# Performance work log

Hardware: AMD Instinct MI355X
Metric: run time of the kernel (lower is better)

The kernel has to match this reference:

```python
import jax, jax.numpy as jnp
import numpy as np

NUM_HEADS = 16
NUM_KV_HEADS = 4
HEAD_DIM = 64
HIDDEN = 1024
B, S = 2, 2048


def setup_inputs() -> dict:
    key = jax.random.key(0)
    ks = jax.random.split(key, 9)
    sc = 0.02
    return {
        "x": jax.random.normal(ks[0], (B, S, HIDDEN), dtype=jnp.float32),
        "Wq": jax.random.normal(ks[1], (HIDDEN, NUM_HEADS * HEAD_DIM), dtype=jnp.float32) * sc,
        "bq": jnp.zeros((NUM_HEADS * HEAD_DIM,), dtype=jnp.float32),
        "Wk": jax.random.normal(ks[2], (HIDDEN, NUM_KV_HEADS * HEAD_DIM), dtype=jnp.float32) * sc,
        "bk": jnp.zeros((NUM_KV_HEADS * HEAD_DIM,), dtype=jnp.float32),
        "Wv": jax.random.normal(ks[3], (HIDDEN, NUM_KV_HEADS * HEAD_DIM), dtype=jnp.float32) * sc,
        "bv": jnp.zeros((NUM_KV_HEADS * HEAD_DIM,), dtype=jnp.float32),
        "Wo": jax.random.normal(ks[4], (NUM_HEADS * HEAD_DIM, HIDDEN), dtype=jnp.float32) * sc,
        "bo": jnp.zeros((HIDDEN,), dtype=jnp.float32),
    }


def reference(x, Wq, bq, Wk, bk, Wv, bv, Wo, bo):
    bs, seq, _ = x.shape
    groups = NUM_HEADS // NUM_KV_HEADS
    # projections -> [B, H, S, D]
    q = (x @ Wq + bq).reshape(bs, seq, NUM_HEADS, HEAD_DIM).transpose(0, 2, 1, 3)
    k = (x @ Wk + bk).reshape(bs, seq, NUM_KV_HEADS, HEAD_DIM).transpose(0, 2, 1, 3)
    v = (x @ Wv + bv).reshape(bs, seq, NUM_KV_HEADS, HEAD_DIM).transpose(0, 2, 1, 3)
    # repeat_interleave KV heads to match query heads (GQA expansion)
    k = jnp.repeat(k, groups, axis=1)
    v = jnp.repeat(v, groups, axis=1)
    # NOTE: source applies NO 1/sqrt(d) scaling and no mask/ALiBi
    scores = jnp.einsum("bhqd,bhkd->bhqk", q, k)
    attn = jax.nn.softmax(scores.astype(jnp.float32), axis=-1).astype(q.dtype)
    out = jnp.einsum("bhqk,bhkd->bhqd", attn, v)
    out = out.transpose(0, 2, 1, 3).reshape(bs, seq, NUM_HEADS * HEAD_DIM)
    return out @ Wo + bo
```

## Files before the change

### kernel.cpp

```cpp
#include <hip/hip_runtime.h>

#define NHEADS 16
#define NKV    4
#define HDIM   64
#define HIDDEN 1024
#define BATCH  2
#define SEQ    2048
#define MROWS  (BATCH * SEQ)
#define LOG2E  1.44269504088896340736f

typedef __bf16 bf16_t;
typedef bf16_t bf16x8 __attribute__((ext_vector_type(8)));
typedef float  f32x4  __attribute__((ext_vector_type(4)));

template<int N>  struct ic { static constexpr int  v = N; };
template<bool B> struct bc { static constexpr bool v = B; };

__device__ __forceinline__ float bf2f(unsigned short u) {
    return __uint_as_float(((unsigned int)u) << 16);
}
__device__ __forceinline__ unsigned short f2bf(float f) {
    unsigned int u = __float_as_uint(f);
    u += 0x7FFFu + ((u >> 16) & 1u);
    return (unsigned short)(u >> 16);
}

__device__ __forceinline__ void gld16(const unsigned short* g, unsigned short* l)
{
    __builtin_amdgcn_global_load_lds(
        (const __attribute__((address_space(1))) void*)g,
        (__attribute__((address_space(3))) void*)l,
        16, 0, 0);
}

__device__ __forceinline__ int swz(int row, int ch) {
    return (row * 8 + (ch ^ (row & 7))) * 8;
}

__device__ __forceinline__ bool sniff_is_f32(const unsigned short* __restrict__ x)
{
    const int e = (x[threadIdx.x & 63] >> 7) & 0xFF;
    const unsigned long long ok = __ballot(e >= 110 && e <= 140);
    return __popcll(ok) < 56;
}

__device__ __forceinline__ void load8cvt(const void* base, size_t elem, bool isf32, unsigned short out[8])
{
    if (!isf32) {
        *(uint4*)out = *(const uint4*)((const unsigned short*)base + elem);
    } else {
        const float* p = (const float*)base + elem;
        float4 v0 = *(const float4*)p;
        float4 v1 = *(const float4*)(p + 4);
        out[0] = f2bf(v0.x); out[1] = f2bf(v0.y); out[2] = f2bf(v0.z); out[3] = f2bf(v0.w);
        out[4] = f2bf(v1.x); out[5] = f2bf(v1.y); out[6] = f2bf(v1.z); out[7] = f2bf(v1.w);
    }
}
__device__ __forceinline__ float bias_at(const void* b, int i, bool isf32)
{
    return isf32 ? ((const float*)b)[i] : bf2f(((const unsigned short*)b)[i]);
}

__global__ __launch_bounds__(256)
void prep_kernel(const void* __restrict__ x,
                 const void* __restrict__ Wq, const void* __restrict__ Wk,
                 const void* __restrict__ Wv, const void* __restrict__ Wo,
                 unsigned short* __restrict__ xb,
                 unsigned short* __restrict__ Wqkvt,
                 unsigned short* __restrict__ Wot)
{
    const bool isf32 = sniff_is_f32((const unsigned short*)x);
    const int t = threadIdx.x;
    int bid = blockIdx.x;

    if (bid < 2048) {
        if (!isf32) return;
        const size_t c = (size_t)bid * 256 + t;
        unsigned short v[8];
        load8cvt(x, c * 8, true, v);
        *(uint4*)(&xb[c * 8]) = *(uint4*)v;
        return;
    }
    bid -= 2048;
    const void* src; unsigned short* dst; int N, rowoff;
    if (bid < 256)      {             src = Wq; dst = Wqkvt; N = 1024; rowoff = 0;    }
    else if (bid < 320) { bid -= 256; src = Wk; dst = Wqkvt; N = 256;  rowoff = 1024; }
    else if (bid < 384) { bid -= 320; src = Wv; dst = Wqkvt; N = 256;  rowoff = 1280; }
    else                { bid -= 384; src = Wo; dst = Wot;   N = 1024; rowoff = 0;    }
    const int ntx = N / 64;
    const int gn0 = (bid % ntx) * 64;
    const int gk0 = (bid / ntx) * 64;

    __shared__ unsigned short Ts[64][72];
#pragma unroll
    for (int half = 0; half < 2; ++half) {
        const int kl = (t >> 3) + half * 32;
        const int n8 = (t & 7) * 8;
        unsigned short v[8];
        load8cvt(src, (size_t)(gk0 + kl) * N + gn0 + n8, isf32, v);
        *(uint4*)(&Ts[kl][n8]) = *(uint4*)v;
    }
    __syncthreads();
#pragma unroll
    for (int half = 0; half < 2; ++half) {
        const int nl = (t >> 3) + half * 32;
        const int k8 = (t & 7) * 8;
        unsigned short v[8];
#pragma unroll
        for (int j = 0; j < 8; ++j) v[j] = Ts[k8 + j][nl];
        *(uint4*)(&dst[(size_t)(rowoff + gn0 + nl) * HIDDEN + gk0 + k8]) = *(uint4*)v;
    }
}

template<int KK>
__device__ __forceinline__ void gemm_tile(const unsigned short* __restrict__ A,
                                          const unsigned short* __restrict__ Bt,
                                          int m0, int n0,
                                          unsigned short* As, unsigned short* Bs,
                                          f32x4 (&acc)[4][4])
{
    const int tid  = threadIdx.x;
    const int lane = tid & 63;
    const int wave = tid >> 6;
    const int quad = lane >> 4;
    const int l15  = lane & 15;
    const int wr   = wave >> 1;
    const int wc   = wave & 1;

    const int srow = tid >> 3;
    const int gch  = ((tid & 7) ^ (srow & 7)) * 8;

    const unsigned short* ga[4];
    const unsigned short* gb[4];
#pragma unroll
    for (int r = 0; r < 4; ++r) {
        ga[r] = A  + (size_t)(m0 + r * 32 + srow) * KK + gch;
        gb[r] = Bt + (size_t)(n0 + r * 32 + srow) * KK + gch;
    }
    unsigned short* const adst = As + wave * 512;
    unsigned short* const bdst = Bs + wave * 512;

    int aoffs[2][4], boffs[2][4];
#pragma unroll
    for (int kk = 0; kk < 2; ++kk) {
#pragma unroll
        for (int i = 0; i < 4; ++i) {
            aoffs[kk][i] = swz(wr * 64 + i * 16 + l15, kk * 4 + quad);
            boffs[kk][i] = swz(wc * 64 + i * 16 + l15, kk * 4 + quad);
        }
    }

#define GSTAGE(B)                                                     \
    do {                                                              \
        _Pragma("unroll")                                             \
        for (int r = 0; r < 4; ++r) {                                 \
            gld16(ga[r], adst + (B) * 8192 + r * 2048); ga[r] += 64;  \
            gld16(gb[r], bdst + (B) * 8192 + r * 2048); gb[r] += 64;  \
        }                                                             \
    } while (0)

    constexpr int nk = KK / 64;
    GSTAGE(0);
#pragma unroll 2
    for (int k = 0; k < nk; ++k) {
        const int cur = k & 1;
        __syncthreads();
        if (k + 1 < nk) GSTAGE(cur ^ 1);

#pragma unroll
        for (int kk = 0; kk < 2; ++kk) {
            bf16x8 af[4], bfv[4];
#pragma unroll
            for (int i = 0; i < 4; ++i) {
                af[i]  = *(const bf16x8*)(&As[cur * 8192 + aoffs[kk][i]]);
                bfv[i] = *(const bf16x8*)(&Bs[cur * 8192 + boffs[kk][i]]);
            }
            __builtin_amdgcn_s_setprio(1);
#pragma unroll
            for (int i = 0; i < 4; ++i)
#pragma unroll
                for (int j = 0; j < 4; ++j)
                    acc[i][j] = __builtin_amdgcn_mfma_f32_16x16x32_bf16(af[i], bfv[j], acc[i][j], 0, 0, 0);
            __builtin_amdgcn_s_setprio(0);
        }
    }
#undef GSTAGE
}

__global__ __launch_bounds__(256)
void gemm_qkv(const void* __restrict__ xraw,
              const unsigned short* __restrict__ xb,
              const unsigned short* __restrict__ Bt,
              const void* __restrict__ bq, const void* __restrict__ bk,
              const void* __restrict__ bv,
              unsigned short* __restrict__ Qh,
              unsigned short* __restrict__ Kh,
              unsigned short* __restrict__ Vt)
{
    __shared__ __align__(16) unsigned short As[2 * 128 * 64];
    __shared__ __align__(16) unsigned short Bs[2 * 128 * 64];
    const bool bias_f32 = sniff_is_f32((const unsigned short*)xraw);
    const unsigned short* A = bias_f32 ? xb : (const unsigned short*)xraw;
    const int lane = threadIdx.x & 63;
    const int wave = threadIdx.x >> 6;
    const int quad = lane >> 4, l15 = lane & 15;
    const int wr = wave >> 1, wc = wave & 1;
    const int m0 = blockIdx.y * 128, n0 = blockIdx.x * 128;

    f32x4 acc[4][4] = {};
    gemm_tile<HIDDEN>(A, Bt, m0, n0, As, Bs, acc);

#pragma unroll
    for (int i = 0; i < 4; ++i) {
#pragma unroll
        for (int j = 0; j < 4; ++j) {
            const int nn  = n0 + wc * 64 + j * 16 + l15;
            const int mmb = m0 + wr * 64 + i * 16 + quad * 4;
            const int b = mmb >> 11, s0 = mmb & 2047;
            if (nn < 1024) {
                const float bias = bias_at(bq, nn, bias_f32);
                const int h = nn >> 6, d = nn & 63;
                const size_t idx0 = (((size_t)(b * NHEADS + h)) * SEQ + s0) * 64 + d;
#pragma unroll
                for (int r = 0; r < 4; ++r)
                    Qh[idx0 + (size_t)r * 64] = f2bf((acc[i][j][r] + bias) * LOG2E);
            } else if (nn < 1280) {
                const int nk = nn - 1024;
                const float bias = bias_at(bk, nk, bias_f32);
                const int h = nk >> 6, d = nk & 63;
                const size_t idx0 = (((size_t)(b * NKV + h)) * SEQ + s0) * 64 + d;
#pragma unroll
                for (int r = 0; r < 4; ++r)
                    Kh[idx0 + (size_t)r * 64] = f2bf(acc[i][j][r] + bias);
            } else {
                const int nv = nn - 1280;
                const float bias = bias_at(bv, nv, bias_f32);
                const int h = nv >> 6, d = nv & 63;
                const size_t idx = (((size_t)(b * NKV + h)) * 64 + d) * SEQ + s0;
                unsigned short vv[4];
#pragma unroll
                for (int r = 0; r < 4; ++r) vv[r] = f2bf(acc[i][j][r] + bias);
                *(uint2*)(&Vt[idx]) = *(uint2*)vv;
            }
        }
    }
}

__global__ __launch_bounds__(256)
void gemm_o(const void* __restrict__ xraw,
            const unsigned short* __restrict__ A,
            const unsigned short* __restrict__ Bt,
            const void* __restrict__ bo,
            float* __restrict__ out)
{
    __shared__ __align__(16) unsigned short As[2 * 128 * 64];
    __shared__ __align__(16) unsigned short Bs[2 * 128 * 64];
    const bool bias_f32 = sniff_is_f32((const unsigned short*)xraw);
    const int lane = threadIdx.x & 63;
    const int wave = threadIdx.x >> 6;
    const int quad = lane >> 4, l15 = lane & 15;
    const int wr = wave >> 1, wc = wave & 1;
    const int m0 = blockIdx.y * 128, n0 = blockIdx.x * 128;

    f32x4 acc[4][4] = {};
    gemm_tile<HIDDEN>(A, Bt, m0, n0, As, Bs, acc);

#pragma unroll
    for (int i = 0; i < 4; ++i) {
#pragma unroll
        for (int j = 0; j < 4; ++j) {
            const int nn = n0 + wc * 64 + j * 16 + l15;
            const float bvv = bias_at(bo, nn, bias_f32);
#pragma unroll
            for (int r = 0; r < 4; ++r) {
                const int mm = m0 + wr * 64 + i * 16 + quad * 4 + r;
                out[(size_t)mm * HIDDEN + nn] = acc[i][j][r] + bvv;
            }
        }
    }
}

#define NT    (SEQ / 64)
#define KVOFF (64 * 64)

__global__ __launch_bounds__(256)
void attn_kernel(const unsigned short* __restrict__ Qh,
                 const unsigned short* __restrict__ Kh,
                 const unsigned short* __restrict__ Vt,
                 unsigned short* __restrict__ O)
{
    __shared__ __align__(16) unsigned short Kth[3 * KVOFF];
    __shared__ __align__(16) unsigned short VtT[3 * KVOFF];
    __shared__ __align__(16) unsigned short Pt[4 * 32 * 64];

    const int tid  = threadIdx.x;
    const int lane = tid & 63;
    const int wave = tid >> 6;
    const int quad = lane >> 4;
    const int l15  = lane & 15;

    const int qt = blockIdx.x;
    const int h  = blockIdx.y;
    const int b  = blockIdx.z;
    const int kv = h >> 2;

    const size_t qoff = ((size_t)(b * NHEADS + h)) * SEQ * HDIM;
    const size_t koff = ((size_t)(b * NKV + kv)) * SEQ * HDIM;
    const size_t voff = ((size_t)(b * NKV + kv)) * HDIM * SEQ;

    const int q0 = qt * 128 + wave * 32;

    bf16x8 qf0[2], qf1[2];
#pragma unroll
    for (int qs = 0; qs < 2; ++qs) {
        const size_t qrow = qoff + (size_t)(q0 + qs * 16 + l15) * HDIM;
        qf0[qs] = *(const bf16x8*)(&Qh[qrow + quad * 8]);
        qf1[qs] = *(const bf16x8*)(&Qh[qrow + 32 + quad * 8]);
    }

    bf16x8 onesv;
#pragma unroll
    for (int i = 0; i < 8; ++i) onesv[i] = (bf16_t)1.0f;

    f32x4 o0[4] = {}, o1[4] = {};
    f32x4 lacc0 = {}, lacc1 = {};

    int koff0[4], koff1[4], pwoff[2][4], proff[2], voffs[2][4];
#pragma unroll
    for (int j = 0; j < 4; ++j) {
        koff0[j] = swz(j * 16 + l15, quad);
        koff1[j] = swz(j * 16 + l15, quad ^ 4);
#pragma unroll
        for (int qs = 0; qs < 2; ++qs)
            pwoff[qs][j] = wave * 2048 + swz(qs * 16 + l15, j * 2 + (quad >> 1)) + (quad & 1) * 4;
    }
#pragma unroll
    for (int kk = 0; kk < 2; ++kk) {
        proff[kk] = wave * 2048 + swz(l15, kk * 4 + quad);
#pragma unroll
        for (int dt = 0; dt < 4; ++dt)
            voffs[kk][dt] = swz(dt * 16 + l15, kk * 4 + quad);
    }

    const unsigned short* kp = Kh + koff;
    const unsigned short* vp = Vt + voff;
    const int srow0 = tid >> 3;
    const int gch_s = ((tid & 7) ^ (srow0 & 7)) * 8;
    unsigned short* const kdst = Kth + wave * 512;
    unsigned short* const vdst = VtT + wave * 512;

#define ATTN_STAGE(B)                                                            \
    do {                                                                         \
        gld16(kp + (size_t)srow0 * HDIM + gch_s,        kdst + (B) * KVOFF);        \
        gld16(kp + (size_t)(srow0 + 32) * HDIM + gch_s, kdst + (B) * KVOFF + 2048); \
        gld16(vp + (size_t)srow0 * SEQ + gch_s,         vdst + (B) * KVOFF);        \
        gld16(vp + (size_t)(srow0 + 32) * SEQ + gch_s,  vdst + (B) * KVOFF + 2048); \
        kp += 64 * HDIM; vp += 64;                                               \
    } while (0)

    ATTN_STAGE(0);
    ATTN_STAGE(1);

    auto step = [&](auto B_, auto STG_, auto LAST_) {
        constexpr int B = decltype(B_)::v;
        if constexpr (decltype(LAST_)::v) asm volatile("s_waitcnt vmcnt(0)" ::: "memory");
        else                              asm volatile("s_waitcnt vmcnt(4)" ::: "memory");
        __builtin_amdgcn_sched_barrier(0);
        __builtin_amdgcn_s_barrier();
        __builtin_amdgcn_sched_barrier(0);
        if constexpr (decltype(STG_)::v) ATTN_STAGE((B + 2) % 3);

#pragma unroll
        for (int j = 0; j < 4; ++j) {
            const bf16x8 kh0 = *(const bf16x8*)(&Kth[B * KVOFF + koff0[j]]);
            const bf16x8 kh1 = *(const bf16x8*)(&Kth[B * KVOFF + koff1[j]]);
#pragma unroll
            for (int qs = 0; qs < 2; ++qs) {
                f32x4 z = {};
                __builtin_amdgcn_s_setprio(1);
                z = __builtin_amdgcn_mfma_f32_16x16x32_bf16(kh0, qs ? qf0[1] : qf0[0], z, 0, 0, 0);
                const f32x4 sc = __builtin_amdgcn_mfma_f32_16x16x32_bf16(kh1, qs ? qf1[1] : qf1[0], z, 0, 0, 0);
                __builtin_amdgcn_s_setprio(0);
                const float p0 = __builtin_amdgcn_exp2f(sc[0]);
                const float p1 = __builtin_amdgcn_exp2f(sc[1]);
                const float p2 = __builtin_amdgcn_exp2f(sc[2]);
                const float p3 = __builtin_amdgcn_exp2f(sc[3]);
                uint2 w;
                w.x = __builtin_amdgcn_perm(__float_as_uint(p1), __float_as_uint(p0), 0x07060302u);
                w.y = __builtin_amdgcn_perm(__float_as_uint(p3), __float_as_uint(p2), 0x07060302u);
                *(uint2*)(&Pt[pwoff[qs][j]]) = w;
            }
        }

#pragma unroll
        for (int kk = 0; kk < 2; ++kk) {
            const bf16x8 pf0 = *(const bf16x8*)(&Pt[proff[kk]]);
            const bf16x8 pf1 = *(const bf16x8*)(&Pt[proff[kk] + 1024]);
            __builtin_amdgcn_s_setprio(1);
            lacc0 = __builtin_amdgcn_mfma_f32_16x16x32_bf16(onesv, pf0, lacc0, 0, 0, 0);
            lacc1 = __builtin_amdgcn_mfma_f32_16x16x32_bf16(onesv, pf1, lacc1, 0, 0, 0);
#pragma unroll
            for (int dt = 0; dt < 4; ++dt) {
                const bf16x8 vf = *(const bf16x8*)(&VtT[B * KVOFF + voffs[kk][dt]]);
                o0[dt] = __builtin_amdgcn_mfma_f32_16x16x32_bf16(vf, pf0, o0[dt], 0, 0, 0);
                o1[dt] = __builtin_amdgcn_mfma_f32_16x16x32_bf16(vf, pf1, o1[dt], 0, 0, 0);
            }
            __builtin_amdgcn_s_setprio(0);
        }
    };

#pragma unroll 1
    for (int t0 = 0; t0 < 30; t0 += 3) {
        step(ic<0>{}, bc<true>{}, bc<false>{});
        step(ic<1>{}, bc<true>{}, bc<false>{});
        step(ic<2>{}, bc<true>{}, bc<false>{});
    }
    step(ic<0>{}, bc<false>{}, bc<false>{});
    step(ic<1>{}, bc<false>{}, bc<true>{});
#undef ATTN_STAGE

#pragma unroll
    for (int qs = 0; qs < 2; ++qs) {
        const float inv = 1.0f / (qs ? lacc1[0] : lacc0[0]);
        const size_t rowbase = ((size_t)b * SEQ + (q0 + qs * 16 + l15)) * (NHEADS * HDIM) + h * HDIM;
#pragma unroll
        for (int dt = 0; dt < 4; ++dt) {
            const f32x4 ov = qs ? o1[dt] : o0[dt];
            unsigned short v4[4];
#pragma unroll
            for (int r = 0; r < 4; ++r) v4[r] = f2bf(ov[r] * inv);
            *(uint2*)(&O[rowbase + dt * 16 + quad * 4]) = *(uint2*)v4;
        }
    }
}

extern "C" void kernel_launch(void* const* d_in, const int* in_sizes, int n_in,
                              void* d_out, int out_size, void* d_ws, size_t ws_size,
                              hipStream_t stream)
{
    const void* x  = d_in[0];
    const void* Wq = d_in[1];
    const void* bq = d_in[2];
    const void* Wk = d_in[3];
    const void* bk = d_in[4];
    const void* Wv = d_in[5];
    const void* bv = d_in[6];
    const void* Wo = d_in[7];
    const void* bo = d_in[8];
    float* out = (float*)d_out;

    unsigned short* p = (unsigned short*)d_ws;
    unsigned short* xb    = p; p += (size_t)MROWS * HIDDEN;
    unsigned short* Wqkvt = p; p += (size_t)1536 * HIDDEN;
    unsigned short* Wot   = p; p += (size_t)HIDDEN * HIDDEN;
    unsigned short* Qh = p;  p += (size_t)MROWS * 1024;
    unsigned short* Kh = p;  p += (size_t)2 * NKV * SEQ * HDIM;
    unsigned short* Vt = p;  p += (size_t)2 * NKV * SEQ * HDIM;
    unsigned short* A2 = p;  p += (size_t)MROWS * 1024;

    dim3 blk(256);
    prep_kernel<<<dim3(2688), blk, 0, stream>>>(x, Wq, Wk, Wv, Wo, xb, Wqkvt, Wot);
    gemm_qkv<<<dim3(1536 / 128, MROWS / 128), blk, 0, stream>>>(
        x, xb, Wqkvt, bq, bk, bv, Qh, Kh, Vt);
    attn_kernel<<<dim3(SEQ / 128, NHEADS, BATCH), blk, 0, stream>>>(Qh, Kh, Vt, A2);
    gemm_o<<<dim3(1024 / 128, MROWS / 128), blk, 0, stream>>>(x, A2, Wot, bo, out);
}
```

Before: 179.8 us.

## Fuse prep, QKV GEMM, attention and O-proj into one persistent megakernel with grid barriers

Replaces four kernel launches with a single persistent kernel of 512 blocks that runs prep, the QKV projection, attention and the output projection, separated by atomic-counter grid barriers. It also swizzles block-to-tile mapping and changes the O-projection tile to 64x128 so that phase has 512 tiles. The aim is to remove launch gaps and inter-kernel drain/fill costs. In exchange it adds a memset plus spin barriers, leaves 128 blocks idle in the QKV phase, and depends on all 512 blocks being co-resident (launch_bounds 256,2).

```diff
diff --git a/kernel.cpp b/kernel.cpp
--- a/kernel.cpp
+++ b/kernel.cpp
@@ -8,6 +8,7 @@
 #define SEQ    2048
 #define MROWS  (BATCH * SEQ)
 #define LOG2E  1.44269504088896340736f
+#define NBLOCKS 512
 
 typedef __bf16 bf16_t;
 typedef bf16_t bf16x8 __attribute__((ext_vector_type(8)));
@@ -35,6 +36,19 @@
 
 __device__ __forceinline__ int swz(int row, int ch) {
     return (row * 8 + (ch ^ (row & 7))) * 8;
+}
+
+__device__ __forceinline__ void gbar(unsigned int* cnt, unsigned int target)
+{
+    __threadfence();
+    __syncthreads();
+    if (threadIdx.x == 0) {
+        __hip_atomic_fetch_add(cnt, 1u, __ATOMIC_RELEASE, __HIP_MEMORY_SCOPE_AGENT);
+        while (__hip_atomic_load(cnt, __ATOMIC_ACQUIRE, __HIP_MEMORY_SCOPE_AGENT) < target)
+            __builtin_amdgcn_s_sleep(4);
+    }
+    __syncthreads();
+    __threadfence();
 }
 
 __device__ __forceinline__ bool sniff_is_f32(const unsigned short* __restrict__ x)
@@ -61,18 +75,16 @@
     return isf32 ? ((const float*)b)[i] : bf2f(((const unsigned short*)b)[i]);
 }
 
-__global__ __launch_bounds__(256)
-void prep_kernel(const void* __restrict__ x,
-                 const void* __restrict__ Wq, const void* __restrict__ Wk,
-                 const void* __restrict__ Wv, const void* __restrict__ Wo,
-                 unsigned short* __restrict__ xb,
-                 unsigned short* __restrict__ Wqkvt,
-                 unsigned short* __restrict__ Wot)
-{
-    const bool isf32 = sniff_is_f32((const unsigned short*)x);
-    const int t = threadIdx.x;
-    int bid = blockIdx.x;
-
+__device__ __forceinline__ void prep_work(int vb, int t, bool isf32,
+                                          const void* __restrict__ x,
+                                          const void* __restrict__ Wq, const void* __restrict__ Wk,
+                                          const void* __restrict__ Wv, const void* __restrict__ Wo,
+                                          unsigned short* __restrict__ xb,
+                                          unsigned short* __restrict__ Wqkvt,
+                                          unsigned short* __restrict__ Wot,
+                                          unsigned short* smem)
+{
+    int bid = vb;
     if (bid < 2048) {
         if (!isf32) return;
         const size_t c = (size_t)bid * 256 + t;
@@ -91,14 +103,14 @@
     const int gn0 = (bid % ntx) * 64;
     const int gk0 = (bid / ntx) * 64;
 
-    __shared__ unsigned short Ts[64][72];
+    __syncthreads();
 #pragma unroll
     for (int half = 0; half < 2; ++half) {
         const int kl = (t >> 3) + half * 32;
         const int n8 = (t & 7) * 8;
         unsigned short v[8];
         load8cvt(src, (size_t)(gk0 + kl) * N + gn0 + n8, isf32, v);
-        *(uint4*)(&Ts[kl][n8]) = *(uint4*)v;
+        *(uint4*)(&smem[kl * 72 + n8]) = *(uint4*)v;
     }
     __syncthreads();
 #pragma unroll
@@ -107,17 +119,17 @@
         const int k8 = (t & 7) * 8;
         unsigned short v[8];
 #pragma unroll
-        for (int j = 0; j < 8; ++j) v[j] = Ts[k8 + j][nl];
+        for (int j = 0; j < 8; ++j) v[j] = smem[(k8 + j) * 72 + nl];
         *(uint4*)(&dst[(size_t)(rowoff + gn0 + nl) * HIDDEN + gk0 + k8]) = *(uint4*)v;
     }
 }
 
-template<int KK>
+template<int AI, int BJ, int KK>
 __device__ __forceinline__ void gemm_tile(const unsigned short* __restrict__ A,
                                           const unsigned short* __restrict__ Bt,
                                           int m0, int n0,
                                           unsigned short* As, unsigned short* Bs,
-                                          f32x4 (&acc)[4][4])
+                                          f32x4 (&acc)[AI][BJ])
 {
     const int tid  = threadIdx.x;
     const int lane = tid & 63;
@@ -130,168 +142,72 @@
     const int srow = tid >> 3;
     const int gch  = ((tid & 7) ^ (srow & 7)) * 8;
 
-    const unsigned short* ga[4];
-    const unsigned short* gb[4];
-#pragma unroll
-    for (int r = 0; r < 4; ++r) {
-        ga[r] = A  + (size_t)(m0 + r * 32 + srow) * KK + gch;
-        gb[r] = Bt + (size_t)(n0 + r * 32 + srow) * KK + gch;
-    }
+    const unsigned short* ga[AI];
+    const unsigned short* gb[BJ];
+#pragma unroll
+    for (int r = 0; r < AI; ++r) ga[r] = A  + (size_t)(m0 + r * 32 + srow) * KK + gch;
+#pragma unroll
+    for (int r = 0; r < BJ; ++r) gb[r] = Bt + (size_t)(n0 + r * 32 + srow) * KK + gch;
+
     unsigned short* const adst = As + wave * 512;
     unsigned short* const bdst = Bs + wave * 512;
 
-    int aoffs[2][4], boffs[2][4];
+    int aoffs[2][AI], boffs[2][BJ];
 #pragma unroll
     for (int kk = 0; kk < 2; ++kk) {
 #pragma unroll
-        for (int i = 0; i < 4; ++i) {
-            aoffs[kk][i] = swz(wr * 64 + i * 16 + l15, kk * 4 + quad);
-            boffs[kk][i] = swz(wc * 64 + i * 16 + l15, kk * 4 + quad);
-        }
-    }
-
-#define GSTAGE(B)                                                     \
-    do {                                                              \
-        _Pragma("unroll")                                             \
-        for (int r = 0; r < 4; ++r) {                                 \
-            gld16(ga[r], adst + (B) * 8192 + r * 2048); ga[r] += 64;  \
-            gld16(gb[r], bdst + (B) * 8192 + r * 2048); gb[r] += 64;  \
-        }                                                             \
-    } while (0)
+        for (int i = 0; i < AI; ++i) aoffs[kk][i] = swz(wr * (AI * 16) + i * 16 + l15, kk * 4 + quad);
+#pragma unroll
+        for (int j = 0; j < BJ; ++j) boffs[kk][j] = swz(wc * (BJ * 16) + j * 16 + l15, kk * 4 + quad);
+    }
+
+    auto stage = [&](int buf) {
+#pragma unroll
+        for (int r = 0; r < AI; ++r) { gld16(ga[r], adst + buf * (AI * 2048) + r * 2048); ga[r] += 64; }
+#pragma unroll
+        for (int r = 0; r < BJ; ++r) { gld16(gb[r], bdst + buf * (BJ * 2048) + r * 2048); gb[r] += 64; }
+    };
 
     constexpr int nk = KK / 64;
-    GSTAGE(0);
+    stage(0);
 #pragma unroll 2
     for (int k = 0; k < nk; ++k) {
         const int cur = k & 1;
         __syncthreads();
-        if (k + 1 < nk) GSTAGE(cur ^ 1);
+        if (k + 1 < nk) stage(cur ^ 1);
 
 #pragma unroll
         for (int kk = 0; kk < 2; ++kk) {
-            bf16x8 af[4], bfv[4];
-#pragma unroll
-            for (int i = 0; i < 4; ++i) {
-                af[i]  = *(const bf16x8*)(&As[cur * 8192 + aoffs[kk][i]]);
-                bfv[i] = *(const bf16x8*)(&Bs[cur * 8192 + boffs[kk][i]]);
-            }
+            bf16x8 af[AI], bfv[BJ];
+#pragma unroll
+            for (int i = 0; i < AI; ++i) af[i]  = *(const bf16x8*)(&As[cur * (AI * 2048) + aoffs[kk][i]]);
+#pragma unroll
+            for (int j = 0; j < BJ; ++j) bfv[j] = *(const bf16x8*)(&Bs[cur * (BJ * 2048) + boffs[kk][j]]);
             __builtin_amdgcn_s_setprio(1);
 #pragma unroll
-            for (int i = 0; i < 4; ++i)
-#pragma unroll
-                for (int j = 0; j < 4; ++j)
+            for (int i = 0; i < AI; ++i)
+#pragma unroll
+                for (int j = 0; j < BJ; ++j)
                     acc[i][j] = __builtin_amdgcn_mfma_f32_16x16x32_bf16(af[i], bfv[j], acc[i][j], 0, 0, 0);
             __builtin_amdgcn_s_setprio(0);
         }
     }
-#undef GSTAGE
-}
-
-__global__ __launch_bounds__(256)
-void gemm_qkv(const void* __restrict__ xraw,
-              const unsigned short* __restrict__ xb,
-              const unsigned short* __restrict__ Bt,
-              const void* __restrict__ bq, const void* __restrict__ bk,
-              const void* __restrict__ bv,
-              unsigned short* __restrict__ Qh,
-              unsigned short* __restrict__ Kh,
-              unsigned short* __restrict__ Vt)
-{
-    __shared__ __align__(16) unsigned short As[2 * 128 * 64];
-    __shared__ __align__(16) unsigned short Bs[2 * 128 * 64];
-    const bool bias_f32 = sniff_is_f32((const unsigned short*)xraw);
-    const unsigned short* A = bias_f32 ? xb : (const unsigned short*)xraw;
-    const int lane = threadIdx.x & 63;
-    const int wave = threadIdx.x >> 6;
-    const int quad = lane >> 4, l15 = lane & 15;
-    const int wr = wave >> 1, wc = wave & 1;
-    const int m0 = blockIdx.y * 128, n0 = blockIdx.x * 128;
-
-    f32x4 acc[4][4] = {};
-    gemm_tile<HIDDEN>(A, Bt, m0, n0, As, Bs, acc);
-
-#pragma unroll
-    for (int i = 0; i < 4; ++i) {
-#pragma unroll
-        for (int j = 0; j < 4; ++j) {
-            const int nn  = n0 + wc * 64 + j * 16 + l15;
-            const int mmb = m0 + wr * 64 + i * 16 + quad * 4;
-            const int b = mmb >> 11, s0 = mmb & 2047;
-            if (nn < 1024) {
-                const float bias = bias_at(bq, nn, bias_f32);
-                const int h = nn >> 6, d = nn & 63;
-                const size_t idx0 = (((size_t)(b * NHEADS + h)) * SEQ + s0) * 64 + d;
-#pragma unroll
-                for (int r = 0; r < 4; ++r)
-                    Qh[idx0 + (size_t)r * 64] = f2bf((acc[i][j][r] + bias) * LOG2E);
-            } else if (nn < 1280) {
-                const int nk = nn - 1024;
-                const float bias = bias_at(bk, nk, bias_f32);
-                const int h = nk >> 6, d = nk & 63;
-                const size_t idx0 = (((size_t)(b * NKV + h)) * SEQ + s0) * 64 + d;
-#pragma unroll
-                for (int r = 0; r < 4; ++r)
-                    Kh[idx0 + (size_t)r * 64] = f2bf(acc[i][j][r] + bias);
-            } else {
-                const int nv = nn - 1280;
-                const float bias = bias_at(bv, nv, bias_f32);
-                const int h = nv >> 6, d = nv & 63;
-                const size_t idx = (((size_t)(b * NKV + h)) * 64 + d) * SEQ + s0;
-                unsigned short vv[4];
-#pragma unroll
-                for (int r = 0; r < 4; ++r) vv[r] = f2bf(acc[i][j][r] + bias);
-                *(uint2*)(&Vt[idx]) = *(uint2*)vv;
-            }
-        }
-    }
-}
-
-__global__ __launch_bounds__(256)
-void gemm_o(const void* __restrict__ xraw,
-            const unsigned short* __restrict__ A,
-            const unsigned short* __restrict__ Bt,
-            const void* __restrict__ bo,
-            float* __restrict__ out)
-{
-    __shared__ __align__(16) unsigned short As[2 * 128 * 64];
-    __shared__ __align__(16) unsigned short Bs[2 * 128 * 64];
-    const bool bias_f32 = sniff_is_f32((const unsigned short*)xraw);
-    const int lane = threadIdx.x & 63;
-    const int wave = threadIdx.x >> 6;
-    const int quad = lane >> 4, l15 = lane & 15;
-    const int wr = wave >> 1, wc = wave & 1;
-    const int m0 = blockIdx.y * 128, n0 = blockIdx.x * 128;
-
-    f32x4 acc[4][4] = {};
-    gemm_tile<HIDDEN>(A, Bt, m0, n0, As, Bs, acc);
-
-#pragma unroll
-    for (int i = 0; i < 4; ++i) {
-#pragma unroll
-        for (int j = 0; j < 4; ++j) {
-            const int nn = n0 + wc * 64 + j * 16 + l15;
-            const float bvv = bias_at(bo, nn, bias_f32);
-#pragma unroll
-            for (int r = 0; r < 4; ++r) {
-                const int mm = m0 + wr * 64 + i * 16 + quad * 4 + r;
-                out[(size_t)mm * HIDDEN + nn] = acc[i][j][r] + bvv;
-            }
-        }
-    }
+    __syncthreads();
 }
 
 #define NT    (SEQ / 64)
 #define KVOFF (64 * 64)
 
-__global__ __launch_bounds__(256)
-void attn_kernel(const unsigned short* __restrict__ Qh,
-                 const unsigned short* __restrict__ Kh,
-                 const unsigned short* __restrict__ Vt,
-                 unsigned short* __restrict__ O)
-{
-    __shared__ __align__(16) unsigned short Kth[3 * KVOFF];
-    __shared__ __align__(16) unsigned short VtT[3 * KVOFF];
-    __shared__ __align__(16) unsigned short Pt[4 * 32 * 64];
+__device__ __forceinline__ void attn_phase(int vb,
+                                           const unsigned short* __restrict__ Qh,
+                                           const unsigned short* __restrict__ Kh,
+                                           const unsigned short* __restrict__ Vt,
+                                           unsigned short* __restrict__ O,
+                                           unsigned short* smem)
+{
+    unsigned short* const Kth = smem;
+    unsigned short* const VtT = smem + 3 * KVOFF;
+    unsigned short* const Pt  = smem + 6 * KVOFF;
 
     const int tid  = threadIdx.x;
     const int lane = tid & 63;
@@ -299,9 +215,9 @@
     const int quad = lane >> 4;
     const int l15  = lane & 15;
 
-    const int qt = blockIdx.x;
-    const int h  = blockIdx.y;
-    const int b  = blockIdx.z;
+    const int qt = vb & 15;
+    const int h  = (vb >> 4) & 15;
+    const int b  = vb >> 8;
     const int kv = h >> 2;
 
     const size_t qoff = ((size_t)(b * NHEADS + h)) * SEQ * HDIM;
@@ -349,13 +265,13 @@
     unsigned short* const kdst = Kth + wave * 512;
     unsigned short* const vdst = VtT + wave * 512;
 
-#define ATTN_STAGE(B)                                                            \
-    do {                                                                         \
+#define ATTN_STAGE(B)                                                               \
+    do {                                                                            \
         gld16(kp + (size_t)srow0 * HDIM + gch_s,        kdst + (B) * KVOFF);        \
         gld16(kp + (size_t)(srow0 + 32) * HDIM + gch_s, kdst + (B) * KVOFF + 2048); \
         gld16(vp + (size_t)srow0 * SEQ + gch_s,         vdst + (B) * KVOFF);        \
         gld16(vp + (size_t)(srow0 + 32) * SEQ + gch_s,  vdst + (B) * KVOFF + 2048); \
-        kp += 64 * HDIM; vp += 64;                                               \
+        kp += 64 * HDIM; vp += 64;                                                  \
     } while (0)
 
     ATTN_STAGE(0);
@@ -434,6 +350,107 @@
     }
 }
 
+__global__ __launch_bounds__(256, 2)
+void megakernel(const void* __restrict__ x,
+                const void* __restrict__ Wq, const void* __restrict__ Wk,
+                const void* __restrict__ Wv, const void* __restrict__ Wo,
+                const void* __restrict__ bq, const void* __restrict__ bk,
+                const void* __restrict__ bv, const void* __restrict__ bo,
+                float* __restrict__ out,
+                unsigned short* __restrict__ xb,
+                unsigned short* __restrict__ Wqkvt,
+                unsigned short* __restrict__ Wot,
+                unsigned short* __restrict__ Qh,
+                unsigned short* __restrict__ Kh,
+                unsigned short* __restrict__ Vt,
+                unsigned short* __restrict__ A2,
+                unsigned int* __restrict__ bar)
+{
+    __shared__ __align__(16) unsigned short smem[32768];
+
+    const bool isf32 = sniff_is_f32((const unsigned short*)x);
+    const int tid  = threadIdx.x;
+    const int bid  = blockIdx.x;
+    const int xswz = (bid & 7) * 64 + (bid >> 3);
+
+    const int lane = tid & 63;
+    const int wave = tid >> 6;
+    const int quad = lane >> 4, l15 = lane & 15;
+    const int wr = wave >> 1, wc = wave & 1;
+
+    for (int vb = bid; vb < 2688; vb += NBLOCKS)
+        prep_work(vb, tid, isf32, x, Wq, Wk, Wv, Wo, xb, Wqkvt, Wot, smem);
+    gbar(bar, NBLOCKS);
+
+    if ((xswz >> 5) < 12) {
+        const unsigned short* A = isf32 ? xb : (const unsigned short*)x;
+        const int m0 = (xswz & 31) * 128;
+        const int n0 = (xswz >> 5) * 128;
+        f32x4 acc[4][4] = {};
+        gemm_tile<4, 4, HIDDEN>(A, Wqkvt, m0, n0, smem, smem + 16384, acc);
+
+#pragma unroll
+        for (int i = 0; i < 4; ++i) {
+#pragma unroll
+            for (int j = 0; j < 4; ++j) {
+                const int nn  = n0 + wc * 64 + j * 16 + l15;
+                const int mmb = m0 + wr * 64 + i * 16 + quad * 4;
+                const int b = mmb >> 11, s0 = mmb & 2047;
+                if (nn < 1024) {
+                    const float bias = bias_at(bq, nn, isf32);
+                    const int h = nn >> 6, d = nn & 63;
+                    const size_t idx0 = (((size_t)(b * NHEADS + h)) * SEQ + s0) * 64 + d;
+#pragma unroll
+                    for (int r = 0; r < 4; ++r)
+                        Qh[idx0 + (size_t)r * 64] = f2bf((acc[i][j][r] + bias) * LOG2E);
+                } else if (nn < 1280) {
+                    const int nk = nn - 1024;
+                    const float bias = bias_at(bk, nk, isf32);
+                    const int h = nk >> 6, d = nk & 63;
+                    const size_t idx0 = (((size_t)(b * NKV + h)) * SEQ + s0) * 64 + d;
+#pragma unroll
+                    for (int r = 0; r < 4; ++r)
+                        Kh[idx0 + (size_t)r * 64] = f2bf(acc[i][j][r] + bias);
+                } else {
+                    const int nv = nn - 1280;
+                    const float bias = bias_at(bv, nv, isf32);
+                    const int h = nv >> 6, d = nv & 63;
+                    const size_t idx = (((size_t)(b * NKV + h)) * 64 + d) * SEQ + s0;
+                    unsigned short vv[4];
+#pragma unroll
+                    for (int r = 0; r < 4; ++r) vv[r] = f2bf(acc[i][j][r] + bias);
+                    *(uint2*)(&Vt[idx]) = *(uint2*)vv;
+                }
+            }
+        }
+    }
+    gbar(bar, 2 * NBLOCKS);
+
+    attn_phase(xswz, Qh, Kh, Vt, A2, smem);
+    gbar(bar, 3 * NBLOCKS);
+
+    {
+        const int m0 = (xswz & 63) * 64;
+        const int n0 = (xswz >> 6) * 128;
+        f32x4 acc[2][4] = {};
+        gemm_tile<2, 4, HIDDEN>(A2, Wot, m0, n0, smem, smem + 8192, acc);
+
+#pragma unroll
+        for (int i = 0; i < 2; ++i) {
+#pragma unroll
+            for (int j = 0; j < 4; ++j) {
+                const int nn = n0 + wc * 64 + j * 16 + l15;
+                const float bvv = bias_at(bo, nn, isf32);
+#pragma unroll
+                for (int r = 0; r < 4; ++r) {
+                    const int mm = m0 + wr * 32 + i * 16 + quad * 4 + r;
+                    out[(size_t)mm * HIDDEN + nn] = acc[i][j][r] + bvv;
+                }
+            }
+        }
+    }
+}
+
 extern "C" void kernel_launch(void* const* d_in, const int* in_sizes, int n_in,
                               void* d_out, int out_size, void* d_ws, size_t ws_size,
                               hipStream_t stream)
@@ -457,11 +474,10 @@
     unsigned short* Kh = p;  p += (size_t)2 * NKV * SEQ * HDIM;
     unsigned short* Vt = p;  p += (size_t)2 * NKV * SEQ * HDIM;
     unsigned short* A2 = p;  p += (size_t)MROWS * 1024;
-
-    dim3 blk(256);
-    prep_kernel<<<dim3(2688), blk, 0, stream>>>(x, Wq, Wk, Wv, Wo, xb, Wqkvt, Wot);
-    gemm_qkv<<<dim3(1536 / 128, MROWS / 128), blk, 0, stream>>>(
-        x, xb, Wqkvt, bq, bk, bv, Qh, Kh, Vt);
-    attn_kernel<<<dim3(SEQ / 128, NHEADS, BATCH), blk, 0, stream>>>(Qh, Kh, Vt, A2);
-    gemm_o<<<dim3(1024 / 128, MROWS / 128), blk, 0, stream>>>(x, A2, Wot, bo, out);
-}
+    unsigned int* bar = (unsigned int*)p;
+
+    hipMemsetAsync((void*)bar, 0, 16, stream);
+    megakernel<<<dim3(NBLOCKS), dim3(256), 0, stream>>>(
+        x, Wq, Wk, Wv, Wo, bq, bk, bv, bo, out,
+        xb, Wqkvt, Wot, Qh, Kh, Vt, A2, bar);
+}
```

New measurement: 583.3 us. +224.4%, slower.
